# Performance work log

Hardware: AMD Instinct MI355X
Metric: run time of the kernel (lower is better)

## Reference

```python
import jax, jax.numpy as jnp
import numpy as np

B, T, D, H = 4, 1024, 1024, 16
DH = D // H  # 64


def setup_inputs() -> dict:
    key = jax.random.key(0)
    ks = jax.random.split(key, 9)
    s = 1.0 / np.sqrt(D)
    return {
        "x": jax.random.normal(ks[0], (B, T, D), dtype=jnp.float32),
        "Wq": jax.random.uniform(ks[1], (D, D), jnp.float32, -s, s),
        "bq": jax.random.uniform(ks[2], (D,), jnp.float32, -s, s),
        "Wk": jax.random.uniform(ks[3], (D, D), jnp.float32, -s, s),
        "bk": jax.random.uniform(ks[4], (D,), jnp.float32, -s, s),
        "Wv": jax.random.uniform(ks[5], (D, DH), jnp.float32, -s, s),
        "bv": jax.random.uniform(ks[6], (DH,), jnp.float32, -s, s),
        "Wo": jax.random.uniform(ks[7], (D, D), jnp.float32, -s, s),
        "bo": jax.random.uniform(ks[8], (D,), jnp.float32, -s, s),
    }


def reference(x, Wq, bq, Wk, bk, Wv, bv, Wo, bo):
    # Q, K: [B, H, T, DH]; shared V: [B, T, DH]
    Q = (x @ Wq + bq).reshape(B, T, H, DH).transpose(0, 2, 1, 3)
    K = (x @ Wk + bk).reshape(B, T, H, DH).transpose(0, 2, 1, 3)
    V = x @ Wv + bv  # [B, T, DH]
    scale = DH ** -0.5
    scores = jnp.einsum("bhqd,bhkd->bhqk", Q, K) * scale
    attn = jax.nn.softmax(scores, axis=-1)  # [B, H, T, T]
    # dropout p=0.0 (eval): identity
    out = jnp.einsum("bhqk,bkd->bhqd", attn, V)  # V broadcast across heads
    out = out.transpose(0, 2, 1, 3).reshape(B, T, D)
    out = out @ Wo + bo
    attn_mean = attn.mean(axis=1)  # [B, T, T]
    return out, attn_mean
```

## Files before the change

### kernel.cpp

```cpp
#include <hip/hip_runtime.h>
#include <math.h>

#define B_ 4
#define T_ 1024
#define D_ 1024
#define H_ 16
#define DH_ 64
#define NCAT 2112

typedef unsigned short u16;
typedef unsigned int u32;
typedef __attribute__((ext_vector_type(8))) short bf16x8;
typedef __attribute__((ext_vector_type(4))) float f32x4;

#define SCALE2 0.18033688f
#define LSTR 72

__device__ __forceinline__ u16 bf16rne(float f) {
  u32 u = __float_as_uint(f);
  u32 r = (u + 0x7fffu + ((u >> 16) & 1u)) >> 16;
  return (u16)r;
}
__device__ __forceinline__ float bf16tof(u16 h) {
  return __uint_as_float((u32)h << 16);
}
__device__ __forceinline__ u32 cvtpk(float lo, float hi) {
  u32 r;
  asm("v_cvt_pk_bf16_f32 %0, %1, %2" : "=v"(r) : "v"(lo), "v"(hi));
  return r;
}

__device__ __forceinline__ void gload_lds16(const u16* g, u16* l) {
  __builtin_amdgcn_global_load_lds(
      (const __attribute__((address_space(1))) unsigned int*)g,
      (__attribute__((address_space(3))) unsigned int*)l, 16, 0, 0);
}

__global__ __launch_bounds__(256) void prep(
    const float* __restrict__ x,
    const float* __restrict__ Wq, const float* __restrict__ Wk,
    const float* __restrict__ Wv, const float* __restrict__ Wo,
    const float* __restrict__ bq, const float* __restrict__ bk,
    const float* __restrict__ bv,
    u16* __restrict__ xhi,
    u16* __restrict__ WcThi, u16* __restrict__ WoThi,
    float* __restrict__ bcat) {
  __shared__ float Ws[64][65];
  const int t = threadIdx.x;
  if (blockIdx.x < 2048) {
    size_t i = ((size_t)blockIdx.x * 256 + t) * 8;
    float4 v0 = *(const float4*)&x[i];
    float4 v1 = *(const float4*)&x[i + 4];
    float vv[8] = {v0.x, v0.y, v0.z, v0.w, v1.x, v1.y, v1.z, v1.w};
    u32 uh[4];
#pragma unroll
    for (int j = 0; j < 4; j++)
      uh[j] = (u32)bf16rne(vv[2 * j]) | ((u32)bf16rne(vv[2 * j + 1]) << 16);
    *(uint4*)&xhi[i] = make_uint4(uh[0], uh[1], uh[2], uh[3]);
    return;
  }
  const int blk = blockIdx.x - 2048;
  if (blk == 784) {
    for (int i = t; i < NCAT; i += 256)
      bcat[i] = (i < 1024) ? bq[i] : ((i < 2048) ? bk[i - 1024] : bv[i - 2048]);
    return;
  }
  const float* W;
  u16* Thi;
  int roff, Nw, bx, by;
  if (blk < 256)      { W = Wq; Thi = WcThi; roff = 0;    Nw = 1024; bx = blk & 15;         by = blk >> 4; }
  else if (blk < 512) { W = Wk; Thi = WcThi; roff = 1024; Nw = 1024; bx = (blk - 256) & 15; by = (blk - 256) >> 4; }
  else if (blk < 768) { W = Wo; Thi = WoThi; roff = 0;    Nw = 1024; bx = (blk - 512) & 15; by = (blk - 512) >> 4; }
  else                { W = Wv; Thi = WcThi; roff = 2048; Nw = 64;   bx = 0;                by = blk - 768; }

  const int n0 = bx * 64, k0 = by * 64;
#pragma unroll
  for (int rr = 0; rr < 4; rr++) {
    int r = rr * 16 + (t >> 4);
    int c = (t & 15) * 4;
    float4 v = *(const float4*)&W[(size_t)(k0 + r) * Nw + n0 + c];
    Ws[r][c] = v.x; Ws[r][c + 1] = v.y; Ws[r][c + 2] = v.z; Ws[r][c + 3] = v.w;
  }
  __syncthreads();
  const int n = t >> 2, kc = t & 3;
  u32 uh[8];
#pragma unroll
  for (int j2 = 0; j2 < 8; j2++) {
    u16 h0 = bf16rne(Ws[kc * 16 + j2 * 2 + 0][n]);
    u16 h1 = bf16rne(Ws[kc * 16 + j2 * 2 + 1][n]);
    uh[j2] = (u32)h0 | ((u32)h1 << 16);
  }
  size_t base = (size_t)(roff + n0 + n) * 1024 + k0 + kc * 16;
  *(uint4*)&Thi[base]     = make_uint4(uh[0], uh[1], uh[2], uh[3]);
  *(uint4*)&Thi[base + 8] = make_uint4(uh[4], uh[5], uh[6], uh[7]);
}

template <int TM, bool QKV>
__global__ __launch_bounds__(256) void mfma_gemm(
    const u16* __restrict__ Ahi, const u16* __restrict__ Bhi,
    const float* __restrict__ bias, float* __restrict__ C,
    int Nvalid, int Kd, int ldc, int mx,
    u16* __restrict__ QK, u16* __restrict__ Vt) {
  constexpr int MF = TM / 32;
  constexpr int AC = TM / 64;
  __shared__ u16 Ah[TM][32];
  __shared__ u16 Bh[128][32];
  const int tid = threadIdx.x;
  const int lane = tid & 63, wid = tid >> 6;
  const int wr = wid >> 1, wc = wid & 1;
  const int nb8 = gridDim.x >> 3;
  const int swz = (blockIdx.x & 7) * nb8 + (blockIdx.x >> 3);
  const int m0 = (swz % mx) * TM, n0 = (swz / mx) * 128;
  f32x4 acc[MF][4];
#pragma unroll
  for (int i = 0; i < MF; i++)
#pragma unroll
    for (int j = 0; j < 4; j++) {
      acc[i][j][0] = 0.f; acc[i][j][1] = 0.f;
      acc[i][j][2] = 0.f; acc[i][j][3] = 0.f;
    }
  const int fo = 8 * (lane >> 4);
  const int fr = lane & 15;
  const int srow = lane >> 2;
  const int scol = (lane & 3) * 8;

#pragma unroll 1
  for (int k0 = 0; k0 < Kd; k0 += 32) {
#pragma unroll
    for (int c = 0; c < AC; c++) {
      int chunk = wid * AC + c;
      size_t ga = (size_t)(m0 + chunk * 16 + srow) * Kd + k0 + scol;
      gload_lds16(&Ahi[ga], ((u16*)Ah) + chunk * 512);
    }
#pragma unroll
    for (int c = 0; c < 2; c++) {
      int chunk = wid * 2 + c;
      int grow = n0 + chunk * 16 + srow;
      if (grow >= Nvalid) grow = Nvalid - 1;
      size_t gb = (size_t)grow * Kd + k0 + scol;
      gload_lds16(&Bhi[gb], ((u16*)Bh) + chunk * 512);
    }
    __syncthreads();
    bf16x8 bhf[4];
#pragma unroll
    for (int nf = 0; nf < 4; nf++) {
      int r = wc * 64 + nf * 16 + fr;
      bhf[nf] = *(bf16x8*)&Bh[r][fo];
    }
#pragma unroll
    for (int mf = 0; mf < MF; mf++) {
      int r = wr * (TM / 2) + mf * 16 + fr;
      bf16x8 ahf = *(bf16x8*)&Ah[r][fo];
#pragma unroll
      for (int nf = 0; nf < 4; nf++)
        acc[mf][nf] = __builtin_amdgcn_mfma_f32_16x16x32_bf16(bhf[nf], ahf, acc[mf][nf], 0, 0, 0);
    }
    __syncthreads();
  }
  const int rq = lane >> 4;
#pragma unroll
  for (int mf = 0; mf < MF; mf++) {
    int m = m0 + wr * (TM / 2) + mf * 16 + fr;
#pragma unroll
    for (int nf = 0; nf < 4; nf++) {
      int nb = n0 + wc * 64 + nf * 16 + rq * 4;
      if (nb < Nvalid) {
        float4 b4 = *(const float4*)&bias[nb];
        float v0 = acc[mf][nf][0] + b4.x;
        float v1 = acc[mf][nf][1] + b4.y;
        float v2 = acc[mf][nf][2] + b4.z;
        float v3 = acc[mf][nf][3] + b4.w;
        if constexpr (QKV) {
          if (nb < 1024) {
            v0 *= SCALE2; v1 *= SCALE2; v2 *= SCALE2; v3 *= SCALE2;
            *(uint2*)&QK[(size_t)m * 2048 + nb] =
                make_uint2((u32)bf16rne(v0) | ((u32)bf16rne(v1) << 16),
                           (u32)bf16rne(v2) | ((u32)bf16rne(v3) << 16));
          } else if (nb < 2048) {
            *(uint2*)&QK[(size_t)m * 2048 + nb] =
                make_uint2((u32)bf16rne(v0) | ((u32)bf16rne(v1) << 16),
                           (u32)bf16rne(v2) | ((u32)bf16rne(v3) << 16));
          } else {
            Vt[(size_t)(nb - 2048 + 0) * 4096 + m] = bf16rne(v0);
            Vt[(size_t)(nb - 2048 + 1) * 4096 + m] = bf16rne(v1);
            Vt[(size_t)(nb - 2048 + 2) * 4096 + m] = bf16rne(v2);
            Vt[(size_t)(nb - 2048 + 3) * 4096 + m] = bf16rne(v3);
          }
        } else {
          float4 o; o.x = v0; o.y = v1; o.z = v2; o.w = v3;
          *(float4*)&C[(size_t)m * ldc + nb] = o;
        }
      }
    }
  }
}

__global__ __launch_bounds__(512) void attn_fused_mfma(
    const u16* __restrict__ QK, const u16* __restrict__ Vt,
    float* __restrict__ mrow, float* __restrict__ linv,
    u16* __restrict__ ophi) {
  __shared__ u16 Kh_s[64][LSTR];
  __shared__ u16 Vt_s[64][LSTR];
  __shared__ u16 P_s[8][16][LSTR];
  const int bi0 = blockIdx.x;
  const int bi = (bi0 & 7) * 64 + (bi0 >> 3);
  const int qt = bi & 7, h = (bi >> 3) & 15, b = bi >> 7;
  const int tid = threadIdx.x;
  const int lane = tid & 63, w = tid >> 6;
  const int l15 = lane & 15, g = lane >> 4;
  const int q0 = qt * 128 + w * 16;
  const int sr = tid >> 3, scs = (tid & 7) * 8;
  bf16x8 qh[2];
  {
    size_t qoff = (size_t)(b * T_ + q0 + l15) * 2048 + h * DH_;
    qh[0] = *(const bf16x8*)&QK[qoff + 8 * g];
    qh[1] = *(const bf16x8*)&QK[qoff + 32 + 8 * g];
  }
  float m_run = -1e30f, l_run = 0.f;
  f32x4 acc_o[4];
#pragma unroll
  for (int nf = 0; nf < 4; nf++) {
    acc_o[nf][0] = 0.f; acc_o[nf][1] = 0.f; acc_o[nf][2] = 0.f; acc_o[nf][3] = 0.f;
  }

  uint4 kreg, vreg;
#define LOAD_TILE(kt_)                                                        \
  {                                                                           \
    kreg = *(const uint4*)&QK[(size_t)(b * T_ + (kt_) * 64 + sr) * 2048 + 1024 + h * DH_ + scs]; \
    vreg = *(const uint4*)&Vt[(size_t)sr * 4096 + b * T_ + (kt_) * 64 + scs]; \
  }
#define STORE_TILE()                                                          \
  {                                                                           \
    *(uint4*)&Kh_s[sr][scs] = kreg;                                           \
    *(uint4*)&Vt_s[sr][scs] = vreg;                                           \
  }

  LOAD_TILE(0);

#pragma unroll 1
  for (int kt = 0; kt < 16; kt++) {
    STORE_TILE();
    __syncthreads();
    if (kt < 15) LOAD_TILE(kt + 1);
    f32x4 accs[4];
#pragma unroll
    for (int mf = 0; mf < 4; mf++) {
      accs[mf][0] = 0.f; accs[mf][1] = 0.f; accs[mf][2] = 0.f; accs[mf][3] = 0.f;
    }
    __builtin_amdgcn_s_setprio(1);
#pragma unroll
    for (int mf = 0; mf < 4; mf++) {
#pragma unroll
      for (int ks = 0; ks < 2; ks++) {
        bf16x8 kh = *(bf16x8*)&Kh_s[mf * 16 + l15][ks * 32 + 8 * g];
        accs[mf] = __builtin_amdgcn_mfma_f32_16x16x32_bf16(kh, qh[ks], accs[mf], 0, 0, 0);
      }
    }
    __builtin_amdgcn_s_setprio(0);
    float t0 = fmaxf(fmaxf(accs[0][0], accs[0][1]), fmaxf(accs[0][2], accs[0][3]));
    float t1 = fmaxf(fmaxf(accs[1][0], accs[1][1]), fmaxf(accs[1][2], accs[1][3]));
    float t2 = fmaxf(fmaxf(accs[2][0], accs[2][1]), fmaxf(accs[2][2], accs[2][3]));
    float t3 = fmaxf(fmaxf(accs[3][0], accs[3][1]), fmaxf(accs[3][2], accs[3][3]));
    float tm = fmaxf(fmaxf(t0, t1), fmaxf(t2, t3));
    tm = fmaxf(tm, __shfl_xor(tm, 16));
    tm = fmaxf(tm, __shfl_xor(tm, 32));
    if (!__all(tm <= m_run + 8.f)) {
      float m_new = fmaxf(m_run, tm);
      float crs = __builtin_amdgcn_exp2f(m_run - m_new);
      l_run *= crs;
#pragma unroll
      for (int nf = 0; nf < 4; nf++)
#pragma unroll
        for (int r = 0; r < 4; r++) acc_o[nf][r] *= crs;
      m_run = m_new;
    }
    float ts = 0.f;
#pragma unroll
    for (int mf = 0; mf < 4; mf++) {
      float p0 = __builtin_amdgcn_exp2f(accs[mf][0] - m_run);
      float p1 = __builtin_amdgcn_exp2f(accs[mf][1] - m_run);
      float p2 = __builtin_amdgcn_exp2f(accs[mf][2] - m_run);
      float p3 = __builtin_amdgcn_exp2f(accs[mf][3] - m_run);
      ts += (p0 + p1) + (p2 + p3);
      *(uint2*)&P_s[w][l15][16 * mf + 4 * g] =
          make_uint2(cvtpk(p0, p1), cvtpk(p2, p3));
    }
    ts += __shfl_xor(ts, 16);
    ts += __shfl_xor(ts, 32);
    l_run += ts;
    bf16x8 pa[2];
    pa[0] = *(bf16x8*)&P_s[w][l15][8 * g];
    pa[1] = *(bf16x8*)&P_s[w][l15][32 + 8 * g];
    __builtin_amdgcn_s_setprio(1);
#pragma unroll
    for (int nf = 0; nf < 4; nf++) {
#pragma unroll
      for (int ks = 0; ks < 2; ks++) {
        bf16x8 vb = *(bf16x8*)&Vt_s[nf * 16 + l15][ks * 32 + 8 * g];
        acc_o[nf] = __builtin_amdgcn_mfma_f32_16x16x32_bf16(vb, pa[ks], acc_o[nf], 0, 0, 0);
      }
    }
    __builtin_amdgcn_s_setprio(0);
    __syncthreads();
  }
#undef LOAD_TILE
#undef STORE_TILE
  float li = 1.0f / l_run;
  if (g == 0) {
    int idx = (b * H_ + h) * T_ + q0 + l15;
    mrow[idx] = m_run;
    linv[idx] = li;
  }
  size_t obase = (size_t)(b * T_ + q0 + l15) * D_ + h * DH_;
#pragma unroll
  for (int nf = 0; nf < 4; nf++) {
    float v0 = acc_o[nf][0] * li, v1 = acc_o[nf][1] * li;
    float v2 = acc_o[nf][2] * li, v3 = acc_o[nf][3] * li;
    *(uint2*)&ophi[obase + nf * 16 + 4 * g] =
        make_uint2((u32)bf16rne(v0) | ((u32)bf16rne(v1) << 16),
                   (u32)bf16rne(v2) | ((u32)bf16rne(v3) << 16));
  }
}

__global__ __launch_bounds__(256) void attn_mean_mfma(
    const u16* __restrict__ QK, const float* __restrict__ mrow,
    const float* __restrict__ linv, float* __restrict__ am_out) {
  __shared__ u16 Kh_s[64][LSTR];
  const int bi0 = blockIdx.x;
  const int bi = (bi0 & 7) * 128 + (bi0 >> 3);
  const int kc = bi & 15, qt = (bi >> 4) & 15, b = bi >> 8;
  const int tid = threadIdx.x;
  const int lane = tid & 63, w = tid >> 6;
  const int l15 = lane & 15, g = lane >> 4;
  const int q0 = qt * 64 + w * 16, k0 = kc * 64;
  const int sr = tid >> 2, scs = (tid & 3) * 16;
  float am[4][4] = {};
  uint4 kreg0, kreg1;
  bf16x8 qhc0, qhc1, qhn0, qhn1;
#define LOAD_K(h_)                                                            \
  {                                                                           \
    size_t krow = (size_t)(b * T_ + k0 + sr) * 2048 + 1024 + (h_) * DH_ + scs; \
    kreg0 = *(const uint4*)&QK[krow];                                         \
    kreg1 = *(const uint4*)&QK[krow + 8];                                     \
  }
#define LOAD_Q(h_, d0, d1)                                                    \
  {                                                                           \
    size_t qoff = (size_t)(b * T_ + q0 + l15) * 2048 + (h_) * DH_;            \
    d0 = *(const bf16x8*)&QK[qoff + 8 * g];                                   \
    d1 = *(const bf16x8*)&QK[qoff + 32 + 8 * g];                              \
  }
  LOAD_K(0);
  LOAD_Q(0, qhc0, qhc1);
#pragma unroll 1
  for (int h = 0; h < H_; h++) {
    *(uint4*)&Kh_s[sr][scs]     = kreg0;
    *(uint4*)&Kh_s[sr][scs + 8] = kreg1;
    __syncthreads();
    if (h < 15) { LOAD_K(h + 1); LOAD_Q(h + 1, qhn0, qhn1); }
    f32x4 accs[4];
#pragma unroll
    for (int mf = 0; mf < 4; mf++) {
      accs[mf][0] = 0.f; accs[mf][1] = 0.f; accs[mf][2] = 0.f; accs[mf][3] = 0.f;
    }
#pragma unroll
    for (int mf = 0; mf < 4; mf++) {
      bf16x8 kh0 = *(bf16x8*)&Kh_s[mf * 16 + l15][8 * g];
      bf16x8 kh1 = *(bf16x8*)&Kh_s[mf * 16 + l15][32 + 8 * g];
      accs[mf] = __builtin_amdgcn_mfma_f32_16x16x32_bf16(kh0, qhc0, accs[mf], 0, 0, 0);
      accs[mf] = __builtin_amdgcn_mfma_f32_16x16x32_bf16(kh1, qhc1, accs[mf], 0, 0, 0);
    }
    const float mq = mrow[(b * H_ + h) * T_ + q0 + l15];
    const float li = linv[(b * H_ + h) * T_ + q0 + l15];
#pragma unroll
    for (int mf = 0; mf < 4; mf++)
#pragma unroll
      for (int r = 0; r < 4; r++)
        am[mf][r] += __builtin_amdgcn_exp2f(accs[mf][r] - mq) * li;
    __syncthreads();
    qhc0 = qhn0; qhc1 = qhn1;
  }
#undef LOAD_K
#undef LOAD_Q
  const float inv16 = 1.0f / 16.0f;
#pragma unroll
  for (int mf = 0; mf < 4; mf++) {
    float4 o;
    o.x = am[mf][0] * inv16; o.y = am[mf][1] * inv16;
    o.z = am[mf][2] * inv16; o.w = am[mf][3] * inv16;
    *(float4*)&am_out[(size_t)(b * T_ + q0 + l15) * T_ + k0 + 16 * mf + 4 * g] = o;
  }
}

extern "C" void kernel_launch(void* const* d_in, const int* in_sizes, int n_in,
                              void* d_out, int out_size, void* d_ws, size_t ws_size,
                              hipStream_t stream) {
  const float* x  = (const float*)d_in[0];
  const float* Wq = (const float*)d_in[1];
  const float* bq = (const float*)d_in[2];
  const float* Wk = (const float*)d_in[3];
  const float* bk = (const float*)d_in[4];
  const float* Wv = (const float*)d_in[5];
  const float* bv = (const float*)d_in[6];
  const float* Wo = (const float*)d_in[7];
  const float* bo = (const float*)d_in[8];

  float* out = (float*)d_out;
  float* am  = out + (size_t)B_ * T_ * D_;

  char* w = (char*)d_ws;
  u16* QK    = (u16*)w; w += (size_t)4096 * 2048 * 2;
  u16* Vt    = (u16*)w; w += (size_t)64 * 4096 * 2;
  u16* xhi   = (u16*)w; w += (size_t)4096 * 1024 * 2;
  u16* WcThi = (u16*)w; w += (size_t)NCAT * 1024 * 2;
  u16* WoThi = (u16*)w; w += (size_t)1024 * 1024 * 2;
  float* mrow  = (float*)w; w += (size_t)B_ * H_ * T_ * 4;
  float* linvp = (float*)w; w += (size_t)B_ * H_ * T_ * 4;
  float* bcat  = (float*)w; w += (size_t)NCAT * 4;

  prep<<<2833, 256, 0, stream>>>(x, Wq, Wk, Wv, Wo, bq, bk, bv,
                                 xhi, WcThi, WoThi, bcat);

  mfma_gemm<128, true><<<544, 256, 0, stream>>>(
      xhi, WcThi, bcat, nullptr, NCAT, 1024, 0, 32, QK, Vt);

  attn_fused_mfma<<<512, 512, 0, stream>>>(QK, Vt, mrow, linvp, xhi);
  attn_mean_mfma<<<1024, 256, 0, stream>>>(QK, mrow, linvp, am);

  mfma_gemm<64, false><<<512, 256, 0, stream>>>(
      xhi, WoThi, bo, out, 1024, 1024, 1024, 64, nullptr, nullptr);
}
```

Baseline: 136.2 us.

## Merge output projection GEMM and attention-mean into one heterogeneous tail launch

```diff
diff --git a/kernel.cpp b/kernel.cpp
--- a/kernel.cpp
+++ b/kernel.cpp
@@ -95,25 +95,22 @@
   *(uint4*)&Thi[base + 8] = make_uint4(uh[4], uh[5], uh[6], uh[7]);
 }
 
-template <int TM, bool QKV>
-__global__ __launch_bounds__(256) void mfma_gemm(
+__global__ __launch_bounds__(256) void mfma_gemm_qkv(
     const u16* __restrict__ Ahi, const u16* __restrict__ Bhi,
-    const float* __restrict__ bias, float* __restrict__ C,
-    int Nvalid, int Kd, int ldc, int mx,
+    const float* __restrict__ bias,
     u16* __restrict__ QK, u16* __restrict__ Vt) {
-  constexpr int MF = TM / 32;
-  constexpr int AC = TM / 64;
-  __shared__ u16 Ah[TM][32];
+  __shared__ u16 Ah[128][32];
   __shared__ u16 Bh[128][32];
   const int tid = threadIdx.x;
   const int lane = tid & 63, wid = tid >> 6;
   const int wr = wid >> 1, wc = wid & 1;
-  const int nb8 = gridDim.x >> 3;
+  const int nb8 = 544 >> 3;
   const int swz = (blockIdx.x & 7) * nb8 + (blockIdx.x >> 3);
-  const int m0 = (swz % mx) * TM, n0 = (swz / mx) * 128;
-  f32x4 acc[MF][4];
-#pragma unroll
-  for (int i = 0; i < MF; i++)
+  const int m0 = (swz % 32) * 128, n0 = (swz / 32) * 128;
+  const int Kd = 1024, Nvalid = NCAT;
+  f32x4 acc[4][4];
+#pragma unroll
+  for (int i = 0; i < 4; i++)
 #pragma unroll
     for (int j = 0; j < 4; j++) {
       acc[i][j][0] = 0.f; acc[i][j][1] = 0.f;
@@ -127,14 +124,10 @@
 #pragma unroll 1
   for (int k0 = 0; k0 < Kd; k0 += 32) {
 #pragma unroll
-    for (int c = 0; c < AC; c++) {
-      int chunk = wid * AC + c;
+    for (int c = 0; c < 2; c++) {
+      int chunk = wid * 2 + c;
       size_t ga = (size_t)(m0 + chunk * 16 + srow) * Kd + k0 + scol;
       gload_lds16(&Ahi[ga], ((u16*)Ah) + chunk * 512);
-    }
-#pragma unroll
-    for (int c = 0; c < 2; c++) {
-      int chunk = wid * 2 + c;
       int grow = n0 + chunk * 16 + srow;
       if (grow >= Nvalid) grow = Nvalid - 1;
       size_t gb = (size_t)grow * Kd + k0 + scol;
@@ -148,8 +141,8 @@
       bhf[nf] = *(bf16x8*)&Bh[r][fo];
     }
 #pragma unroll
-    for (int mf = 0; mf < MF; mf++) {
-      int r = wr * (TM / 2) + mf * 16 + fr;
+    for (int mf = 0; mf < 4; mf++) {
+      int r = wr * 64 + mf * 16 + fr;
       bf16x8 ahf = *(bf16x8*)&Ah[r][fo];
 #pragma unroll
       for (int nf = 0; nf < 4; nf++)
@@ -159,8 +152,8 @@
   }
   const int rq = lane >> 4;
 #pragma unroll
-  for (int mf = 0; mf < MF; mf++) {
-    int m = m0 + wr * (TM / 2) + mf * 16 + fr;
+  for (int mf = 0; mf < 4; mf++) {
+    int m = m0 + wr * 64 + mf * 16 + fr;
 #pragma unroll
     for (int nf = 0; nf < 4; nf++) {
       int nb = n0 + wc * 64 + nf * 16 + rq * 4;
@@ -170,25 +163,20 @@
         float v1 = acc[mf][nf][1] + b4.y;
         float v2 = acc[mf][nf][2] + b4.z;
         float v3 = acc[mf][nf][3] + b4.w;
-        if constexpr (QKV) {
-          if (nb < 1024) {
-            v0 *= SCALE2; v1 *= SCALE2; v2 *= SCALE2; v3 *= SCALE2;
-            *(uint2*)&QK[(size_t)m * 2048 + nb] =
-                make_uint2((u32)bf16rne(v0) | ((u32)bf16rne(v1) << 16),
-                           (u32)bf16rne(v2) | ((u32)bf16rne(v3) << 16));
-          } else if (nb < 2048) {
-            *(uint2*)&QK[(size_t)m * 2048 + nb] =
-                make_uint2((u32)bf16rne(v0) | ((u32)bf16rne(v1) << 16),
-                           (u32)bf16rne(v2) | ((u32)bf16rne(v3) << 16));
-          } else {
-            Vt[(size_t)(nb - 2048 + 0) * 4096 + m] = bf16rne(v0);
-            Vt[(size_t)(nb - 2048 + 1) * 4096 + m] = bf16rne(v1);
-            Vt[(size_t)(nb - 2048 + 2) * 4096 + m] = bf16rne(v2);
-            Vt[(size_t)(nb - 2048 + 3) * 4096 + m] = bf16rne(v3);
-          }
+        if (nb < 1024) {
+          v0 *= SCALE2; v1 *= SCALE2; v2 *= SCALE2; v3 *= SCALE2;
+          *(uint2*)&QK[(size_t)m * 2048 + nb] =
+              make_uint2((u32)bf16rne(v0) | ((u32)bf16rne(v1) << 16),
+                         (u32)bf16rne(v2) | ((u32)bf16rne(v3) << 16));
+        } else if (nb < 2048) {
+          *(uint2*)&QK[(size_t)m * 2048 + nb] =
+              make_uint2((u32)bf16rne(v0) | ((u32)bf16rne(v1) << 16),
+                         (u32)bf16rne(v2) | ((u32)bf16rne(v3) << 16));
         } else {
-          float4 o; o.x = v0; o.y = v1; o.z = v2; o.w = v3;
-          *(float4*)&C[(size_t)m * ldc + nb] = o;
+          Vt[(size_t)(nb - 2048 + 0) * 4096 + m] = bf16rne(v0);
+          Vt[(size_t)(nb - 2048 + 1) * 4096 + m] = bf16rne(v1);
+          Vt[(size_t)(nb - 2048 + 2) * 4096 + m] = bf16rne(v2);
+          Vt[(size_t)(nb - 2048 + 3) * 4096 + m] = bf16rne(v3);
         }
       }
     }
@@ -322,72 +310,143 @@
   }
 }
 
-__global__ __launch_bounds__(256) void attn_mean_mfma(
+__global__ __launch_bounds__(256) void tail(
+    const u16* __restrict__ xhi, const u16* __restrict__ WoThi,
+    const float* __restrict__ bo, float* __restrict__ out,
     const u16* __restrict__ QK, const float* __restrict__ mrow,
     const float* __restrict__ linv, float* __restrict__ am_out) {
-  __shared__ u16 Kh_s[64][LSTR];
-  const int bi0 = blockIdx.x;
-  const int bi = (bi0 & 7) * 128 + (bi0 >> 3);
-  const int kc = bi & 15, qt = (bi >> 4) & 15, b = bi >> 8;
+  __shared__ u16 pool[64 * 32 + 128 * 32];
   const int tid = threadIdx.x;
-  const int lane = tid & 63, w = tid >> 6;
+  const int lane = tid & 63, w4 = tid >> 6;
   const int l15 = lane & 15, g = lane >> 4;
-  const int q0 = qt * 64 + w * 16, k0 = kc * 64;
-  const int sr = tid >> 2, scs = (tid & 3) * 16;
-  float am[4][4] = {};
-  uint4 kreg0, kreg1;
-  bf16x8 qhc0, qhc1, qhn0, qhn1;
+
+  if (blockIdx.x < 512) {
+    u16(*Ah)[32] = (u16(*)[32])pool;
+    u16(*Bh)[32] = (u16(*)[32])(pool + 64 * 32);
+    const int wr = w4 >> 1, wc = w4 & 1;
+    const int swz = ((int)blockIdx.x & 7) * 64 + ((int)blockIdx.x >> 3);
+    const int m0 = (swz % 64) * 64, n0 = (swz / 64) * 128;
+    const int Kd = 1024;
+    f32x4 acc[2][4];
+#pragma unroll
+    for (int i = 0; i < 2; i++)
+#pragma unroll
+      for (int j = 0; j < 4; j++) {
+        acc[i][j][0] = 0.f; acc[i][j][1] = 0.f;
+        acc[i][j][2] = 0.f; acc[i][j][3] = 0.f;
+      }
+    const int fo = 8 * g;
+    const int fr = l15;
+    const int srow = lane >> 2;
+    const int scol = (lane & 3) * 8;
+#pragma unroll 1
+    for (int k0 = 0; k0 < Kd; k0 += 32) {
+      {
+        int chunk = w4;
+        size_t ga = (size_t)(m0 + chunk * 16 + srow) * Kd + k0 + scol;
+        gload_lds16(&xhi[ga], ((u16*)Ah) + chunk * 512);
+      }
+#pragma unroll
+      for (int c = 0; c < 2; c++) {
+        int chunk = w4 * 2 + c;
+        size_t gb = (size_t)(n0 + chunk * 16 + srow) * Kd + k0 + scol;
+        gload_lds16(&WoThi[gb], ((u16*)Bh) + chunk * 512);
+      }
+      __syncthreads();
+      bf16x8 bhf[4];
+#pragma unroll
+      for (int nf = 0; nf < 4; nf++) {
+        int r = wc * 64 + nf * 16 + fr;
+        bhf[nf] = *(bf16x8*)&Bh[r][fo];
+      }
+#pragma unroll
+      for (int mf = 0; mf < 2; mf++) {
+        int r = wr * 32 + mf * 16 + fr;
+        bf16x8 ahf = *(bf16x8*)&Ah[r][fo];
+#pragma unroll
+        for (int nf = 0; nf < 4; nf++)
+          acc[mf][nf] = __builtin_amdgcn_mfma_f32_16x16x32_bf16(bhf[nf], ahf, acc[mf][nf], 0, 0, 0);
+      }
+      __syncthreads();
+    }
+    const int rq = g;
+#pragma unroll
+    for (int mf = 0; mf < 2; mf++) {
+      int m = m0 + wr * 32 + mf * 16 + fr;
+#pragma unroll
+      for (int nf = 0; nf < 4; nf++) {
+        int nb = n0 + wc * 64 + nf * 16 + rq * 4;
+        float4 b4 = *(const float4*)&bo[nb];
+        float4 o;
+        o.x = acc[mf][nf][0] + b4.x;
+        o.y = acc[mf][nf][1] + b4.y;
+        o.z = acc[mf][nf][2] + b4.z;
+        o.w = acc[mf][nf][3] + b4.w;
+        *(float4*)&out[(size_t)m * 1024 + nb] = o;
+      }
+    }
+  } else {
+    u16(*Kh_s)[LSTR] = (u16(*)[LSTR])pool;
+    const int bi0 = (int)blockIdx.x - 512;
+    const int bi = (bi0 & 7) * 128 + (bi0 >> 3);
+    const int kc = bi & 15, qt = (bi >> 4) & 15, b = bi >> 8;
+    const int q0 = qt * 64 + w4 * 16, k0 = kc * 64;
+    const int sr = tid >> 2, scs = (tid & 3) * 16;
+    float am[4][4] = {};
+    uint4 kreg0, kreg1;
+    bf16x8 qhc0, qhc1, qhn0, qhn1;
 #define LOAD_K(h_)                                                            \
-  {                                                                           \
-    size_t krow = (size_t)(b * T_ + k0 + sr) * 2048 + 1024 + (h_) * DH_ + scs; \
-    kreg0 = *(const uint4*)&QK[krow];                                         \
-    kreg1 = *(const uint4*)&QK[krow + 8];                                     \
-  }
+    {                                                                         \
+      size_t krow = (size_t)(b * T_ + k0 + sr) * 2048 + 1024 + (h_) * DH_ + scs; \
+      kreg0 = *(const uint4*)&QK[krow];                                       \
+      kreg1 = *(const uint4*)&QK[krow + 8];                                   \
+    }
 #define LOAD_Q(h_, d0, d1)                                                    \
-  {                                                                           \
-    size_t qoff = (size_t)(b * T_ + q0 + l15) * 2048 + (h_) * DH_;            \
-    d0 = *(const bf16x8*)&QK[qoff + 8 * g];                                   \
-    d1 = *(const bf16x8*)&QK[qoff + 32 + 8 * g];                              \
-  }
-  LOAD_K(0);
-  LOAD_Q(0, qhc0, qhc1);
+    {                                                                         \
+      size_t qoff = (size_t)(b * T_ + q0 + l15) * 2048 + (h_) * DH_;          \
+      d0 = *(const bf16x8*)&QK[qoff + 8 * g];                                 \
+      d1 = *(const bf16x8*)&QK[qoff + 32 + 8 * g];                            \
+    }
+    LOAD_K(0);
+    LOAD_Q(0, qhc0, qhc1);
 #pragma unroll 1
-  for (int h = 0; h < H_; h++) {
-    *(uint4*)&Kh_s[sr][scs]     = kreg0;
-    *(uint4*)&Kh_s[sr][scs + 8] = kreg1;
-    __syncthreads();
-    if (h < 15) { LOAD_K(h + 1); LOAD_Q(h + 1, qhn0, qhn1); }
-    f32x4 accs[4];
-#pragma unroll
-    for (int mf = 0; mf < 4; mf++) {
-      accs[mf][0] = 0.f; accs[mf][1] = 0.f; accs[mf][2] = 0.f; accs[mf][3] = 0.f;
-    }
-#pragma unroll
-    for (int mf = 0; mf < 4; mf++) {
-      bf16x8 kh0 = *(bf16x8*)&Kh_s[mf * 16 + l15][8 * g];
-      bf16x8 kh1 = *(bf16x8*)&Kh_s[mf * 16 + l15][32 + 8 * g];
-      accs[mf] = __builtin_amdgcn_mfma_f32_16x16x32_bf16(kh0, qhc0, accs[mf], 0, 0, 0);
-      accs[mf] = __builtin_amdgcn_mfma_f32_16x16x32_bf16(kh1, qhc1, accs[mf], 0, 0, 0);
-    }
-    const float mq = mrow[(b * H_ + h) * T_ + q0 + l15];
-    const float li = linv[(b * H_ + h) * T_ + q0 + l15];
-#pragma unroll
-    for (int mf = 0; mf < 4; mf++)
-#pragma unroll
-      for (int r = 0; r < 4; r++)
-        am[mf][r] += __builtin_amdgcn_exp2f(accs[mf][r] - mq) * li;
-    __syncthreads();
-    qhc0 = qhn0; qhc1 = qhn1;
-  }
+    for (int h = 0; h < H_; h++) {
+      *(uint4*)&Kh_s[sr][scs]     = kreg0;
+      *(uint4*)&Kh_s[sr][scs + 8] = kreg1;
+      __syncthreads();
+      if (h < 15) { LOAD_K(h + 1); LOAD_Q(h + 1, qhn0, qhn1); }
+      f32x4 accs[4];
+#pragma unroll
+      for (int mf = 0; mf < 4; mf++) {
+        accs[mf][0] = 0.f; accs[mf][1] = 0.f; accs[mf][2] = 0.f; accs[mf][3] = 0.f;
+      }
+#pragma unroll
+      for (int mf = 0; mf < 4; mf++) {
+        bf16x8 kh0 = *(bf16x8*)&Kh_s[mf * 16 + l15][8 * g];
+        bf16x8 kh1 = *(bf16x8*)&Kh_s[mf * 16 + l15][32 + 8 * g];
+        accs[mf] = __builtin_amdgcn_mfma_f32_16x16x32_bf16(kh0, qhc0, accs[mf], 0, 0, 0);
+        accs[mf] = __builtin_amdgcn_mfma_f32_16x16x32_bf16(kh1, qhc1, accs[mf], 0, 0, 0);
+      }
+      const float mq = mrow[(b * H_ + h) * T_ + q0 + l15];
+      const float li = linv[(b * H_ + h) * T_ + q0 + l15];
+#pragma unroll
+      for (int mf = 0; mf < 4; mf++)
+#pragma unroll
+        for (int r = 0; r < 4; r++)
+          am[mf][r] += __builtin_amdgcn_exp2f(accs[mf][r] - mq) * li;
+      __syncthreads();
+      qhc0 = qhn0; qhc1 = qhn1;
+    }
 #undef LOAD_K
 #undef LOAD_Q
-  const float inv16 = 1.0f / 16.0f;
-#pragma unroll
-  for (int mf = 0; mf < 4; mf++) {
-    float4 o;
-    o.x = am[mf][0] * inv16; o.y = am[mf][1] * inv16;
-    o.z = am[mf][2] * inv16; o.w = am[mf][3] * inv16;
-    *(float4*)&am_out[(size_t)(b * T_ + q0 + l15) * T_ + k0 + 16 * mf + 4 * g] = o;
+    const float inv16 = 1.0f / 16.0f;
+#pragma unroll
+    for (int mf = 0; mf < 4; mf++) {
+      float4 o;
+      o.x = am[mf][0] * inv16; o.y = am[mf][1] * inv16;
+      o.z = am[mf][2] * inv16; o.w = am[mf][3] * inv16;
+      *(float4*)&am_out[(size_t)(b * T_ + q0 + l15) * T_ + k0 + 16 * mf + 4 * g] = o;
+    }
   }
 }
 
@@ -420,12 +479,9 @@
   prep<<<2833, 256, 0, stream>>>(x, Wq, Wk, Wv, Wo, bq, bk, bv,
                                  xhi, WcThi, WoThi, bcat);
 
-  mfma_gemm<128, true><<<544, 256, 0, stream>>>(
-      xhi, WcThi, bcat, nullptr, NCAT, 1024, 0, 32, QK, Vt);
+  mfma_gemm_qkv<<<544, 256, 0, stream>>>(xhi, WcThi, bcat, QK, Vt);
 
   attn_fused_mfma<<<512, 512, 0, stream>>>(QK, Vt, mrow, linvp, xhi);
-  attn_mean_mfma<<<1024, 256, 0, stream>>>(QK, mrow, linvp, am);
-
-  mfma_gemm<64, false><<<512, 256, 0, stream>>>(
-      xhi, WoThi, bo, out, 1024, 1024, 1024, 64, nullptr, nullptr);
-}
+
+  tail<<<1536, 256, 0, stream>>>(xhi, WoThi, bo, out, QK, mrow, linvp, am);
+}
```

Result: faster. 132.2 us, median of 2 (-2.9%).
